# Optimization experiments

Measured on AMD Instinct MI355X. Metric: run time of the kernel, lower is better.

Reference implementation:

```python
import jax, jax.numpy as jnp
import numpy as np

N_NODES = 100000


def gcn_conv(x, W, b, src, tgt, n_nodes):
    """PyG GCNConv: add self-loops, symmetric deg^-1/2 normalization, then aggregate."""
    xw = x @ W  # [N, out]
    # degree including self-loop (edge weights are all 1)
    deg = jnp.zeros((n_nodes,), dtype=x.dtype).at[tgt].add(1.0) + 1.0
    dinv = deg ** -0.5
    norm = dinv[src] * dinv[tgt]  # [E]
    agg = jax.ops.segment_sum(xw[src] * norm[:, None], tgt, num_segments=n_nodes)
    # self-loop contribution: norm_ii = dinv_i^2
    return agg + xw * (dinv ** 2)[:, None] + b


def setup_inputs() -> dict:
    key = jax.random.key(0)
    ks = jax.random.split(key, 9)
    d_in, d_hid, d_out = 128, 128, 64
    x = jax.random.normal(ks[0], (N_NODES, d_in), dtype=jnp.float32)
    edge_index = jax.random.randint(ks[1], (2, 200000), 0, N_NODES)
    pos_edge_index = jax.random.randint(ks[2], (2, 500000), 0, N_NODES)
    s = lambda k, shape, fan: jax.random.normal(k, shape, dtype=jnp.float32) / np.sqrt(fan)
    return {
        "x": x,
        "edge_index": edge_index,
        "pos_edge_index": pos_edge_index,
        "W_init": s(ks[3], (d_in, d_in), d_in),
        "b_init": jnp.zeros((d_in,), dtype=jnp.float32),
        "W1": s(ks[4], (d_in, d_hid), d_in),
        "b1": jnp.zeros((d_hid,), dtype=jnp.float32),
        "W2": s(ks[5], (d_hid, d_out), d_hid),
        "b2": jnp.zeros((d_out,), dtype=jnp.float32),
    }


def reference(x, edge_index, pos_edge_index, W_init, b_init, W1, b1, W2, b2):
    n = x.shape[0]
    src, tgt = pos_edge_index[0], pos_edge_index[1]
    h = x @ W_init + b_init                      # init_linear
    h = gcn_conv(h, W1, b1, src, tgt, n)         # conv1
    h = jax.nn.relu(h)
    h = gcn_conv(h, W2, b2, src, tgt, n)         # conv2
    # edge dot-product scoring (use_bilinear=False)
    logits = jnp.sum(h[edge_index[0]] * h[edge_index[1]], axis=-1)  # [E_pred]
    return logits
```

## Files before the change

### kernel.cpp

```cpp
#include <hip/hip_runtime.h>


typedef __attribute__((ext_vector_type(8))) short short8;
typedef __attribute__((ext_vector_type(4))) float f32x4;

__device__ __forceinline__ ushort f2bf(float v) {
    unsigned u = __float_as_uint(v);
    return (ushort)((u + 0x7FFFu + ((u >> 16) & 1u)) >> 16);
}
__device__ __forceinline__ float bf2f(ushort b) {
    return __uint_as_float(((unsigned)b) << 16);
}
__device__ __forceinline__ void split2(float v, ushort& h, ushort& l) {
    unsigned u = __float_as_uint(v);
    unsigned hb = (u + 0x7FFFu + ((u >> 16) & 1u)) & 0xFFFF0000u;
    h = (ushort)(hb >> 16);
    l = f2bf(v - __uint_as_float(hb));
}

__global__ void zero_ints_kernel(int* __restrict__ p, int n) {
    int i = blockIdx.x * blockDim.x + threadIdx.x;
    if (i < n) p[i] = 0;
}
__global__ void hist_kernel(const int* __restrict__ tgt, int* __restrict__ counts, int e) {
    int i = blockIdx.x * blockDim.x + threadIdx.x;
    if (i < e) atomicAdd(&counts[tgt[i]], 1);
}
__global__ __launch_bounds__(256)
void scan1_kernel(const int* __restrict__ counts, int* __restrict__ rowptr,
                  int* __restrict__ bsum, float* __restrict__ dinv, int n)
{
    __shared__ int sdata[256];
    const int t = threadIdx.x;
    const int base = blockIdx.x * 1024 + t * 4;
    int v[4];
#pragma unroll
    for (int i = 0; i < 4; i++) v[i] = (base + i < n) ? counts[base + i] : 0;
#pragma unroll
    for (int i = 0; i < 4; i++)
        if (base + i < n) dinv[base + i] = 1.0f / sqrtf((float)(v[i] + 1));
    int tsum = v[0] + v[1] + v[2] + v[3];
    sdata[t] = tsum;
    __syncthreads();
    for (int off = 1; off < 256; off <<= 1) {
        int x = (t >= off) ? sdata[t - off] : 0;
        __syncthreads();
        if (t >= off) sdata[t] += x;
        __syncthreads();
    }
    if (t == 255) bsum[blockIdx.x] = sdata[255];
    int run = sdata[t] - tsum;
#pragma unroll
    for (int i = 0; i < 4; i++) {
        if (base + i < n) rowptr[base + i] = run;
        run += v[i];
    }
}
__global__ __launch_bounds__(256)
void scan2_kernel(int* __restrict__ bsum, int nb)
{
    __shared__ int sdata[256];
    const int t = threadIdx.x;
    int v = (t < nb) ? bsum[t] : 0;
    sdata[t] = v;
    __syncthreads();
    for (int off = 1; off < 256; off <<= 1) {
        int x = (t >= off) ? sdata[t - off] : 0;
        __syncthreads();
        if (t >= off) sdata[t] += x;
        __syncthreads();
    }
    if (t < nb) bsum[t] = sdata[t] - v;
}
__global__ void scan3_kernel(int* __restrict__ rowptr, const int* __restrict__ bsum,
                             int n, int e_total)
{
    int i = blockIdx.x * blockDim.x + threadIdx.x;
    if (i < n) rowptr[i] += bsum[i >> 10];
    if (i == 0) rowptr[n] = e_total;
}
__global__ void scatter_kernel(const int* __restrict__ src, const int* __restrict__ tgt,
                               const float* __restrict__ dinv, const int* __restrict__ rowptr,
                               int* __restrict__ cursor, int2* __restrict__ ew, int e)
{
    int i = blockIdx.x * blockDim.x + threadIdx.x;
    if (i >= e) return;
    int s = src[i], t = tgt[i];
    int p = rowptr[t] + atomicAdd(&cursor[t], 1);
    ew[p] = make_int2(s, __float_as_int(dinv[s] * dinv[t]));
}

__global__ void wtrans_all_kernel(const float* __restrict__ Wi, const float* __restrict__ W1,
                                  const float* __restrict__ W2,
                                  ushort* __restrict__ Ti, ushort* __restrict__ T1,
                                  ushort* __restrict__ T2)
{
    int o = blockIdx.x * blockDim.x + threadIdx.x;
    if (o < 16384) {
        int c = o >> 7, k = o & 127;
        Ti[o] = f2bf(Wi[(size_t)k * 128 + c]);
    } else if (o < 32768) {
        int p = o - 16384;
        int c = p >> 7, k = p & 127;
        T1[p] = f2bf(W1[(size_t)k * 128 + c]);
    } else if (o < 40960) {
        int p = o - 32768;
        int c = p >> 7, k = p & 127;
        T2[p] = f2bf(W2[(size_t)k * 64 + c]);
    }
}

__global__ __launch_bounds__(256)
void fused_gemm01_kernel(const float* __restrict__ x,
                         const ushort* __restrict__ WTi, const ushort* __restrict__ WT1,
                         const float* __restrict__ bias, ushort* __restrict__ xw1, int M)
{
    __shared__ ushort raw[36864];
    ushort (*H0h)[128][8] = (ushort(*)[128][8])raw;
    ushort (*H0l)[128][8] = (ushort(*)[128][8])(raw + 16384);
    ushort (*Bs)[128][8]  = (ushort(*)[128][8])(raw + 32768);

    const int tid = threadIdx.x;
    const int row0 = blockIdx.x * 128;
    const int wv = tid >> 6;
    const int l  = tid & 63;
    const int lr = l & 15;
    const int lk = l >> 4;

    f32x4 acc0[8], acc1[8];
#pragma unroll
    for (int n = 0; n < 8; ++n) {
        acc0[n] = (f32x4){0.f, 0.f, 0.f, 0.f};
        acc1[n] = (f32x4){0.f, 0.f, 0.f, 0.f};
    }

    for (int kk = 0; kk < 128; kk += 32) {
        {
            const int r  = tid >> 1;
            const int kh = tid & 1;
            const int gr = row0 + r;
            float f[16];
            if (gr < M) {
                const float4* p = (const float4*)(x + (size_t)gr * 128 + kk + kh * 16);
                float4 q0 = p[0], q1 = p[1], q2 = p[2], q3 = p[3];
                f[0]=q0.x; f[1]=q0.y; f[2]=q0.z; f[3]=q0.w;
                f[4]=q1.x; f[5]=q1.y; f[6]=q1.z; f[7]=q1.w;
                f[8]=q2.x; f[9]=q2.y; f[10]=q2.z; f[11]=q2.w;
                f[12]=q3.x; f[13]=q3.y; f[14]=q3.z; f[15]=q3.w;
            } else {
#pragma unroll
                for (int j = 0; j < 16; j++) f[j] = 0.f;
            }
#pragma unroll
            for (int uu = 0; uu < 2; ++uu) {
                short8 hv, lv;
#pragma unroll
                for (int j = 0; j < 8; ++j) {
                    ushort h, lo;
                    split2(f[8 * uu + j], h, lo);
                    hv[j] = (short)h; lv[j] = (short)lo;
                }
                *(short8*)&H0h[2 * kh + uu][r][0] = hv;
                *(short8*)&H0l[2 * kh + uu][r][0] = lv;
            }
        }
        {
#pragma unroll
            for (int u = 0; u < 2; ++u) {
                const int unit = tid * 2 + u;
                const int c   = unit >> 2;
                const int kgl = unit & 3;
                *(short8*)&Bs[kgl][c][0] = *(const short8*)(WTi + (size_t)c * 128 + kk + 8 * kgl);
            }
        }
        __syncthreads();
        short8 ah0 = *(const short8*)&H0h[lk][wv * 32 + lr][0];
        short8 ah1 = *(const short8*)&H0h[lk][wv * 32 + 16 + lr][0];
        short8 al0 = *(const short8*)&H0l[lk][wv * 32 + lr][0];
        short8 al1 = *(const short8*)&H0l[lk][wv * 32 + 16 + lr][0];
#pragma unroll
        for (int n = 0; n < 8; ++n) {
            short8 bh = *(const short8*)&Bs[lk][n * 16 + lr][0];
            acc0[n] = __builtin_amdgcn_mfma_f32_16x16x32_bf16(bh, ah0, acc0[n], 0, 0, 0);
            acc1[n] = __builtin_amdgcn_mfma_f32_16x16x32_bf16(bh, ah1, acc1[n], 0, 0, 0);
            acc0[n] = __builtin_amdgcn_mfma_f32_16x16x32_bf16(bh, al0, acc0[n], 0, 0, 0);
            acc1[n] = __builtin_amdgcn_mfma_f32_16x16x32_bf16(bh, al1, acc1[n], 0, 0, 0);
        }
        __syncthreads();
    }

#pragma unroll
    for (int n = 0; n < 8; ++n) {
        const float4 b4 = *(const float4*)(bias + n * 16 + 4 * lk);
        const float bb[4] = {b4.x, b4.y, b4.z, b4.w};
        const int ks = 2 * n + (lk >> 1);
        const int jo = (lk & 1) * 4;
#pragma unroll
        for (int half = 0; half < 2; ++half) {
            const int m = wv * 32 + 16 * half + lr;
            uint2 uh, ul;
            unsigned hw[4], lw[4];
#pragma unroll
            for (int r = 0; r < 4; ++r) {
                ushort h, lo;
                split2((half ? acc1[n][r] : acc0[n][r]) + bb[r], h, lo);
                hw[r] = h; lw[r] = lo;
            }
            uh.x = hw[0] | (hw[1] << 16); uh.y = hw[2] | (hw[3] << 16);
            ul.x = lw[0] | (lw[1] << 16); ul.y = lw[2] | (lw[3] << 16);
            *(uint2*)&H0h[ks][m][jo] = uh;
            *(uint2*)&H0l[ks][m][jo] = ul;
        }
    }
    __syncthreads();

#pragma unroll
    for (int n = 0; n < 8; ++n) {
        acc0[n] = (f32x4){0.f, 0.f, 0.f, 0.f};
        acc1[n] = (f32x4){0.f, 0.f, 0.f, 0.f};
    }
    for (int kk = 0; kk < 4; ++kk) {
        {
#pragma unroll
            for (int u = 0; u < 2; ++u) {
                const int unit = tid * 2 + u;
                const int c   = unit >> 2;
                const int kgl = unit & 3;
                *(short8*)&Bs[kgl][c][0] = *(const short8*)(WT1 + (size_t)c * 128 + kk * 32 + 8 * kgl);
            }
        }
        __syncthreads();
        short8 ah0 = *(const short8*)&H0h[kk * 4 + lk][wv * 32 + lr][0];
        short8 ah1 = *(const short8*)&H0h[kk * 4 + lk][wv * 32 + 16 + lr][0];
        short8 al0 = *(const short8*)&H0l[kk * 4 + lk][wv * 32 + lr][0];
        short8 al1 = *(const short8*)&H0l[kk * 4 + lk][wv * 32 + 16 + lr][0];
#pragma unroll
        for (int n = 0; n < 8; ++n) {
            short8 bh = *(const short8*)&Bs[lk][n * 16 + lr][0];
            acc0[n] = __builtin_amdgcn_mfma_f32_16x16x32_bf16(bh, ah0, acc0[n], 0, 0, 0);
            acc1[n] = __builtin_amdgcn_mfma_f32_16x16x32_bf16(bh, ah1, acc1[n], 0, 0, 0);
            acc0[n] = __builtin_amdgcn_mfma_f32_16x16x32_bf16(bh, al0, acc0[n], 0, 0, 0);
            acc1[n] = __builtin_amdgcn_mfma_f32_16x16x32_bf16(bh, al1, acc1[n], 0, 0, 0);
        }
        __syncthreads();
    }

#pragma unroll
    for (int n = 0; n < 8; ++n) {
#pragma unroll
        for (int half = 0; half < 2; ++half) {
            const int m = row0 + wv * 32 + 16 * half + lr;
            if (m < M) {
                uint2 u;
                const f32x4 a = half ? acc1[n] : acc0[n];
                u.x = (unsigned)f2bf(a[0]) | ((unsigned)f2bf(a[1]) << 16);
                u.y = (unsigned)f2bf(a[2]) | ((unsigned)f2bf(a[3]) << 16);
                *(uint2*)(xw1 + (size_t)m * 128 + n * 16 + 4 * lk) = u;
            }
        }
    }
}

__global__ __launch_bounds__(256)
void gemm2_kernel(const ushort* __restrict__ Ap, const ushort* __restrict__ WT2,
                  ushort* __restrict__ xw2, int M)
{
    __shared__ ushort Ah[4][128][8];
    __shared__ ushort Bs[4][64][8];

    const int tid = threadIdx.x;
    const int row0 = blockIdx.x * 128;
    const int wv = tid >> 6;
    const int l  = tid & 63;
    const int lr = l & 15;
    const int lk = l >> 4;

    f32x4 acc0[4], acc1[4];
#pragma unroll
    for (int n = 0; n < 4; ++n) {
        acc0[n] = (f32x4){0.f, 0.f, 0.f, 0.f};
        acc1[n] = (f32x4){0.f, 0.f, 0.f, 0.f};
    }

    for (int kk = 0; kk < 128; kk += 32) {
        {
            const int r  = tid >> 1;
            const int kh = tid & 1;
            const int gr = row0 + r;
            short8 h0, h1;
            if (gr < M) {
                const size_t o = (size_t)gr * 128 + kk + kh * 16;
                h0 = *(const short8*)(Ap + o);
                h1 = *(const short8*)(Ap + o + 8);
            } else {
#pragma unroll
                for (int j = 0; j < 8; j++) { h0[j] = 0; h1[j] = 0; }
            }
            *(short8*)&Ah[2 * kh + 0][r][0] = h0;
            *(short8*)&Ah[2 * kh + 1][r][0] = h1;
        }
        {
            const int c   = tid >> 2;
            const int kgl = tid & 3;
            *(short8*)&Bs[kgl][c][0] = *(const short8*)(WT2 + (size_t)c * 128 + kk + 8 * kgl);
        }
        __syncthreads();
        short8 ah0 = *(const short8*)&Ah[lk][wv * 32 + lr][0];
        short8 ah1 = *(const short8*)&Ah[lk][wv * 32 + 16 + lr][0];
#pragma unroll
        for (int n = 0; n < 4; ++n) {
            short8 bh = *(const short8*)&Bs[lk][n * 16 + lr][0];
            acc0[n] = __builtin_amdgcn_mfma_f32_16x16x32_bf16(bh, ah0, acc0[n], 0, 0, 0);
            acc1[n] = __builtin_amdgcn_mfma_f32_16x16x32_bf16(bh, ah1, acc1[n], 0, 0, 0);
        }
        __syncthreads();
    }

#pragma unroll
    for (int n = 0; n < 4; ++n) {
#pragma unroll
        for (int half = 0; half < 2; ++half) {
            const int m = row0 + wv * 32 + 16 * half + lr;
            if (m < M) {
                uint2 u;
                const f32x4 a = half ? acc1[n] : acc0[n];
                u.x = (unsigned)f2bf(a[0]) | ((unsigned)f2bf(a[1]) << 16);
                u.y = (unsigned)f2bf(a[2]) | ((unsigned)f2bf(a[3]) << 16);
                *(uint2*)(xw2 + (size_t)m * 64 + n * 16 + 4 * lk) = u;
            }
        }
    }
}

__global__ __launch_bounds__(256)
void gather1_kernel(const ushort* __restrict__ xw, const float* __restrict__ dinv,
                    const int* __restrict__ rowptr, const int2* __restrict__ ew,
                    const float* __restrict__ bias, ushort* __restrict__ outp, int n)
{
    const int node = blockIdx.x * 4 + (threadIdx.x >> 6);
    const int lane = threadIdx.x & 63;
    if (node >= n) return;
    const float dt = dinv[node];
    int j = rowptr[node];
    const int j1 = rowptr[node + 1];

    const unsigned self = *(const unsigned*)(xw + (size_t)node * 128 + 2 * lane);
    const float c = dt * dt;
    float accx = fmaf(__uint_as_float(self << 16), c, bias[2 * lane]);
    float accy = fmaf(__uint_as_float(self & 0xFFFF0000u), c, bias[2 * lane + 1]);

    for (; j + 3 < j1; j += 4) {
        const int2 p0 = ew[j], p1 = ew[j + 1], p2 = ew[j + 2], p3 = ew[j + 3];
        const unsigned v0 = *(const unsigned*)(xw + (size_t)p0.x * 128 + 2 * lane);
        const unsigned v1 = *(const unsigned*)(xw + (size_t)p1.x * 128 + 2 * lane);
        const unsigned v2 = *(const unsigned*)(xw + (size_t)p2.x * 128 + 2 * lane);
        const unsigned v3 = *(const unsigned*)(xw + (size_t)p3.x * 128 + 2 * lane);
        const float w0 = __int_as_float(p0.y), w1 = __int_as_float(p1.y);
        const float w2 = __int_as_float(p2.y), w3 = __int_as_float(p3.y);
        accx = fmaf(__uint_as_float(v0 << 16), w0, accx);
        accy = fmaf(__uint_as_float(v0 & 0xFFFF0000u), w0, accy);
        accx = fmaf(__uint_as_float(v1 << 16), w1, accx);
        accy = fmaf(__uint_as_float(v1 & 0xFFFF0000u), w1, accy);
        accx = fmaf(__uint_as_float(v2 << 16), w2, accx);
        accy = fmaf(__uint_as_float(v2 & 0xFFFF0000u), w2, accy);
        accx = fmaf(__uint_as_float(v3 << 16), w3, accx);
        accy = fmaf(__uint_as_float(v3 & 0xFFFF0000u), w3, accy);
    }
    for (; j < j1; ++j) {
        const int2 p0 = ew[j];
        const unsigned v0 = *(const unsigned*)(xw + (size_t)p0.x * 128 + 2 * lane);
        const float w0 = __int_as_float(p0.y);
        accx = fmaf(__uint_as_float(v0 << 16), w0, accx);
        accy = fmaf(__uint_as_float(v0 & 0xFFFF0000u), w0, accy);
    }

    const float rx = fmaxf(accx, 0.f);
    const float ry = fmaxf(accy, 0.f);
    *(unsigned*)(outp + (size_t)node * 128 + 2 * lane) =
        (unsigned)f2bf(rx) | ((unsigned)f2bf(ry) << 16);
}

__global__ __launch_bounds__(256)
void gather2_kernel(const ushort* __restrict__ xw, const float* __restrict__ dinv,
                    const int* __restrict__ rowptr, const int2* __restrict__ ew,
                    const float* __restrict__ bias, ushort* __restrict__ out, int n)
{
    const int node = blockIdx.x * 4 + (threadIdx.x >> 6);
    const int lane = threadIdx.x & 63;
    if (node >= n) return;
    const float dt = dinv[node];
    int j = rowptr[node];
    const int j1 = rowptr[node + 1];

    float acc = fmaf(bf2f(xw[(size_t)node * 64 + lane]), dt * dt, bias[lane]);
    for (; j + 3 < j1; j += 4) {
        const int2 p0 = ew[j], p1 = ew[j + 1], p2 = ew[j + 2], p3 = ew[j + 3];
        const float v0 = bf2f(xw[(size_t)p0.x * 64 + lane]);
        const float v1 = bf2f(xw[(size_t)p1.x * 64 + lane]);
        const float v2 = bf2f(xw[(size_t)p2.x * 64 + lane]);
        const float v3 = bf2f(xw[(size_t)p3.x * 64 + lane]);
        acc = fmaf(v0, __int_as_float(p0.y), acc);
        acc = fmaf(v1, __int_as_float(p1.y), acc);
        acc = fmaf(v2, __int_as_float(p2.y), acc);
        acc = fmaf(v3, __int_as_float(p3.y), acc);
    }
    for (; j < j1; ++j) {
        const int2 p0 = ew[j];
        acc = fmaf(bf2f(xw[(size_t)p0.x * 64 + lane]), __int_as_float(p0.y), acc);
    }
    out[(size_t)node * 64 + lane] = f2bf(acc);
}

__global__ void score_kernel(const ushort* __restrict__ h, const int* __restrict__ ea,
                             const int* __restrict__ eb, float* __restrict__ out, int E)
{
    long long gid = (long long)blockIdx.x * blockDim.x + threadIdx.x;
    int e = (int)(gid >> 3);
    int l = (int)(gid & 7);
    if (e >= E) return;
    int a = ea[e], b = eb[e];
    uint4 ua = *(const uint4*)(h + (size_t)a * 64 + 8 * l);
    uint4 ub = *(const uint4*)(h + (size_t)b * 64 + 8 * l);
    float s;
    s  = __uint_as_float(ua.x << 16)         * __uint_as_float(ub.x << 16);
    s += __uint_as_float(ua.x & 0xFFFF0000u) * __uint_as_float(ub.x & 0xFFFF0000u);
    s += __uint_as_float(ua.y << 16)         * __uint_as_float(ub.y << 16);
    s += __uint_as_float(ua.y & 0xFFFF0000u) * __uint_as_float(ub.y & 0xFFFF0000u);
    s += __uint_as_float(ua.z << 16)         * __uint_as_float(ub.z << 16);
    s += __uint_as_float(ua.z & 0xFFFF0000u) * __uint_as_float(ub.z & 0xFFFF0000u);
    s += __uint_as_float(ua.w << 16)         * __uint_as_float(ub.w << 16);
    s += __uint_as_float(ua.w & 0xFFFF0000u) * __uint_as_float(ub.w & 0xFFFF0000u);
    s += __shfl_xor(s, 4);
    s += __shfl_xor(s, 2);
    s += __shfl_xor(s, 1);
    if (l == 0) out[e] = s;
}

extern "C" void kernel_launch(void* const* d_in, const int* in_sizes, int n_in,
                              void* d_out, int out_size, void* d_ws, size_t ws_size,
                              hipStream_t stream)
{
    const float* x              = (const float*)d_in[0];
    const int*   edge_index     = (const int*)d_in[1];
    const int*   pos_edge_index = (const int*)d_in[2];
    const float* W_init         = (const float*)d_in[3];
    const float* b_init         = (const float*)d_in[4];
    const float* W1             = (const float*)d_in[5];
    const float* b1             = (const float*)d_in[6];
    const float* W2             = (const float*)d_in[7];
    const float* b2             = (const float*)d_in[8];
    float* out = (float*)d_out;

    const int N     = in_sizes[0] / 128;
    const int Epred = in_sizes[1] / 2;
    const int E     = in_sizes[2] / 2;

    const int* src = pos_edge_index;
    const int* tgt = pos_edge_index + E;
    const int* ea  = edge_index;
    const int* eb  = edge_index + Epred;

    int2*   ew   = (int2*)d_ws;
    ushort* regA = (ushort*)(ew + E);
    ushort* regB = regA + (size_t)N * 128;
    float*  dinv = (float*)(regB + (size_t)N * 128);
    int*   counts = (int*)(dinv + N);
    int*   cursor = counts + N;
    int*   rowptr = cursor + N;
    int*   bsum   = rowptr + N + 2;
    ushort* WTi = (ushort*)(((uintptr_t)(bsum + 256) + 15) & ~(uintptr_t)15);
    ushort* WT1 = WTi + 16384;
    ushort* WT2 = WT1 + 16384;

    ushort* xw1 = regA;
    ushort* r1  = regB;
    ushort* xw2 = regA;
    ushort* h2  = regB;

    const int BLK = 256;
    const int nb  = (N + 1023) / 1024;
    const int gemm_grid = (N + 127) / 128;

    zero_ints_kernel<<<(2 * N + BLK - 1) / BLK, BLK, 0, stream>>>(counts, 2 * N);
    hist_kernel<<<(E + BLK - 1) / BLK, BLK, 0, stream>>>(tgt, counts, E);
    scan1_kernel<<<nb, 256, 0, stream>>>(counts, rowptr, bsum, dinv, N);
    scan2_kernel<<<1, 256, 0, stream>>>(bsum, nb);
    scan3_kernel<<<(N + BLK - 1) / BLK, BLK, 0, stream>>>(rowptr, bsum, N, E);
    scatter_kernel<<<(E + BLK - 1) / BLK, BLK, 0, stream>>>(src, tgt, dinv, rowptr, cursor, ew, E);

    wtrans_all_kernel<<<160, BLK, 0, stream>>>(W_init, W1, W2, WTi, WT1, WT2);

    fused_gemm01_kernel<<<gemm_grid, BLK, 0, stream>>>(x, WTi, WT1, b_init, xw1, N);

    gather1_kernel<<<(N + 3) / 4, BLK, 0, stream>>>(xw1, dinv, rowptr, ew, b1, r1, N);

    gemm2_kernel<<<gemm_grid, BLK, 0, stream>>>(r1, WT2, xw2, N);

    gather2_kernel<<<(N + 3) / 4, BLK, 0, stream>>>(xw2, dinv, rowptr, ew, b2, h2, N);

    score_kernel<<<((long long)Epred * 8 + BLK - 1) / BLK, BLK, 0, stream>>>(
        h2, ea, eb, out, Epred);
}
```

Measured before the change: 196.9 us.

## Fuse conv1 gather, ReLU and second GEMM into one tiled kernel

Replaces the separate gather1 and gemm2 kernels with one kernel. Each block of 64 target nodes stages its CSR edges in shared memory and accumulates the neighbour aggregation into a bf16 shared tile. ReLU is applied by zeroing negative bf16 values, and the tile is then multiplied by W2 with MFMA, so the relu'd hidden activations never make a round trip through global memory. It also folds the counter zeroing into the weight-transpose kernel to save a launch. The cost is extra rounding, because per-segment partial sums are added into a bf16 tile, plus a binary search per edge and a slow fallback path for blocks with more than 1536 edges.

Result: faster. 192.6 us (-2.2%).

```diff
diff --git a/kernel.cpp b/kernel.cpp
--- a/kernel.cpp
+++ b/kernel.cpp
@@ -10,6 +10,11 @@
 }
 __device__ __forceinline__ float bf2f(ushort b) {
     return __uint_as_float(((unsigned)b) << 16);
+}
+__device__ __forceinline__ float bflo(unsigned u) { return __uint_as_float(u << 16); }
+__device__ __forceinline__ float bfhi(unsigned u) { return __uint_as_float(u & 0xFFFF0000u); }
+__device__ __forceinline__ unsigned packbf(float x, float y) {
+    return (unsigned)f2bf(x) | ((unsigned)f2bf(y) << 16);
 }
 __device__ __forceinline__ void split2(float v, ushort& h, ushort& l) {
     unsigned u = __float_as_uint(v);
@@ -18,84 +23,13 @@
     l = f2bf(v - __uint_as_float(hb));
 }
 
-__global__ void zero_ints_kernel(int* __restrict__ p, int n) {
-    int i = blockIdx.x * blockDim.x + threadIdx.x;
-    if (i < n) p[i] = 0;
-}
-__global__ void hist_kernel(const int* __restrict__ tgt, int* __restrict__ counts, int e) {
-    int i = blockIdx.x * blockDim.x + threadIdx.x;
-    if (i < e) atomicAdd(&counts[tgt[i]], 1);
-}
-__global__ __launch_bounds__(256)
-void scan1_kernel(const int* __restrict__ counts, int* __restrict__ rowptr,
-                  int* __restrict__ bsum, float* __restrict__ dinv, int n)
-{
-    __shared__ int sdata[256];
-    const int t = threadIdx.x;
-    const int base = blockIdx.x * 1024 + t * 4;
-    int v[4];
-#pragma unroll
-    for (int i = 0; i < 4; i++) v[i] = (base + i < n) ? counts[base + i] : 0;
-#pragma unroll
-    for (int i = 0; i < 4; i++)
-        if (base + i < n) dinv[base + i] = 1.0f / sqrtf((float)(v[i] + 1));
-    int tsum = v[0] + v[1] + v[2] + v[3];
-    sdata[t] = tsum;
-    __syncthreads();
-    for (int off = 1; off < 256; off <<= 1) {
-        int x = (t >= off) ? sdata[t - off] : 0;
-        __syncthreads();
-        if (t >= off) sdata[t] += x;
-        __syncthreads();
-    }
-    if (t == 255) bsum[blockIdx.x] = sdata[255];
-    int run = sdata[t] - tsum;
-#pragma unroll
-    for (int i = 0; i < 4; i++) {
-        if (base + i < n) rowptr[base + i] = run;
-        run += v[i];
-    }
-}
-__global__ __launch_bounds__(256)
-void scan2_kernel(int* __restrict__ bsum, int nb)
-{
-    __shared__ int sdata[256];
-    const int t = threadIdx.x;
-    int v = (t < nb) ? bsum[t] : 0;
-    sdata[t] = v;
-    __syncthreads();
-    for (int off = 1; off < 256; off <<= 1) {
-        int x = (t >= off) ? sdata[t - off] : 0;
-        __syncthreads();
-        if (t >= off) sdata[t] += x;
-        __syncthreads();
-    }
-    if (t < nb) bsum[t] = sdata[t] - v;
-}
-__global__ void scan3_kernel(int* __restrict__ rowptr, const int* __restrict__ bsum,
-                             int n, int e_total)
-{
-    int i = blockIdx.x * blockDim.x + threadIdx.x;
-    if (i < n) rowptr[i] += bsum[i >> 10];
-    if (i == 0) rowptr[n] = e_total;
-}
-__global__ void scatter_kernel(const int* __restrict__ src, const int* __restrict__ tgt,
-                               const float* __restrict__ dinv, const int* __restrict__ rowptr,
-                               int* __restrict__ cursor, int2* __restrict__ ew, int e)
-{
-    int i = blockIdx.x * blockDim.x + threadIdx.x;
-    if (i >= e) return;
-    int s = src[i], t = tgt[i];
-    int p = rowptr[t] + atomicAdd(&cursor[t], 1);
-    ew[p] = make_int2(s, __float_as_int(dinv[s] * dinv[t]));
-}
-
-__global__ void wtrans_all_kernel(const float* __restrict__ Wi, const float* __restrict__ W1,
-                                  const float* __restrict__ W2,
-                                  ushort* __restrict__ Ti, ushort* __restrict__ T1,
-                                  ushort* __restrict__ T2)
+__global__ void prep_kernel(const float* __restrict__ Wi, const float* __restrict__ W1,
+                            const float* __restrict__ W2,
+                            ushort* __restrict__ Ti, ushort* __restrict__ T1,
+                            ushort* __restrict__ T2, int* __restrict__ zp, int ztot)
 {
     int o = blockIdx.x * blockDim.x + threadIdx.x;
+    if (o < ztot) zp[o] = 0;
     if (o < 16384) {
         int c = o >> 7, k = o & 127;
         Ti[o] = f2bf(Wi[(size_t)k * 128 + c]);
@@ -108,6 +42,74 @@
         int c = p >> 7, k = p & 127;
         T2[p] = f2bf(W2[(size_t)k * 64 + c]);
     }
+}
+
+__global__ void hist_kernel(const int* __restrict__ tgt, int* __restrict__ counts, int e) {
+    int i = blockIdx.x * blockDim.x + threadIdx.x;
+    if (i < e) atomicAdd(&counts[tgt[i]], 1);
+}
+__global__ __launch_bounds__(256)
+void scan1_kernel(const int* __restrict__ counts, int* __restrict__ rowptr,
+                  int* __restrict__ bsum, float* __restrict__ dinv, int n)
+{
+    __shared__ int sdata[256];
+    const int t = threadIdx.x;
+    const int base = blockIdx.x * 1024 + t * 4;
+    int v[4];
+#pragma unroll
+    for (int i = 0; i < 4; i++) v[i] = (base + i < n) ? counts[base + i] : 0;
+#pragma unroll
+    for (int i = 0; i < 4; i++)
+        if (base + i < n) dinv[base + i] = 1.0f / sqrtf((float)(v[i] + 1));
+    int tsum = v[0] + v[1] + v[2] + v[3];
+    sdata[t] = tsum;
+    __syncthreads();
+    for (int off = 1; off < 256; off <<= 1) {
+        int x = (t >= off) ? sdata[t - off] : 0;
+        __syncthreads();
+        if (t >= off) sdata[t] += x;
+        __syncthreads();
+    }
+    if (t == 255) bsum[blockIdx.x] = sdata[255];
+    int run = sdata[t] - tsum;
+#pragma unroll
+    for (int i = 0; i < 4; i++) {
+        if (base + i < n) rowptr[base + i] = run;
+        run += v[i];
+    }
+}
+__global__ __launch_bounds__(256)
+void scan2_kernel(int* __restrict__ bsum, int nb)
+{
+    __shared__ int sdata[256];
+    const int t = threadIdx.x;
+    int v = (t < nb) ? bsum[t] : 0;
+    sdata[t] = v;
+    __syncthreads();
+    for (int off = 1; off < 256; off <<= 1) {
+        int x = (t >= off) ? sdata[t - off] : 0;
+        __syncthreads();
+        if (t >= off) sdata[t] += x;
+        __syncthreads();
+    }
+    if (t < nb) bsum[t] = sdata[t] - v;
+}
+__global__ void scan3_kernel(int* __restrict__ rowptr, const int* __restrict__ bsum,
+                             int n, int e_total)
+{
+    int i = blockIdx.x * blockDim.x + threadIdx.x;
+    if (i < n) rowptr[i] += bsum[i >> 10];
+    if (i == 0) rowptr[n] = e_total;
+}
+__global__ void scatter_kernel(const int* __restrict__ src, const int* __restrict__ tgt,
+                               const float* __restrict__ dinv, const int* __restrict__ rowptr,
+                               int* __restrict__ cursor, int2* __restrict__ ew, int e)
+{
+    int i = blockIdx.x * blockDim.x + threadIdx.x;
+    if (i >= e) return;
+    int s = src[i], t = tgt[i];
+    int p = rowptr[t] + atomicAdd(&cursor[t], 1);
+    ew[p] = make_int2(s, __float_as_int(dinv[s] * dinv[t]));
 }
 
 __global__ __launch_bounds__(256)
@@ -261,123 +263,155 @@
     }
 }
 
+#define C1_CAP 1536
+
+__device__ __forceinline__ void tile_add(unsigned* p, float ax, float ay) {
+    unsigned old = *p;
+    *p = packbf(bflo(old) + ax, bfhi(old) + ay);
+}
+
 __global__ __launch_bounds__(256)
-void gemm2_kernel(const ushort* __restrict__ Ap, const ushort* __restrict__ WT2,
-                  ushort* __restrict__ xw2, int M)
-{
-    __shared__ ushort Ah[4][128][8];
-    __shared__ ushort Bs[4][64][8];
-
-    const int tid = threadIdx.x;
-    const int row0 = blockIdx.x * 128;
-    const int wv = tid >> 6;
-    const int l  = tid & 63;
-    const int lr = l & 15;
-    const int lk = l >> 4;
-
-    f32x4 acc0[4], acc1[4];
-#pragma unroll
-    for (int n = 0; n < 4; ++n) {
-        acc0[n] = (f32x4){0.f, 0.f, 0.f, 0.f};
-        acc1[n] = (f32x4){0.f, 0.f, 0.f, 0.f};
-    }
-
-    for (int kk = 0; kk < 128; kk += 32) {
-        {
-            const int r  = tid >> 1;
-            const int kh = tid & 1;
-            const int gr = row0 + r;
-            short8 h0, h1;
-            if (gr < M) {
-                const size_t o = (size_t)gr * 128 + kk + kh * 16;
-                h0 = *(const short8*)(Ap + o);
-                h1 = *(const short8*)(Ap + o + 8);
-            } else {
-#pragma unroll
-                for (int j = 0; j < 8; j++) { h0[j] = 0; h1[j] = 0; }
-            }
-            *(short8*)&Ah[2 * kh + 0][r][0] = h0;
-            *(short8*)&Ah[2 * kh + 1][r][0] = h1;
-        }
-        {
-            const int c   = tid >> 2;
-            const int kgl = tid & 3;
-            *(short8*)&Bs[kgl][c][0] = *(const short8*)(WT2 + (size_t)c * 128 + kk + 8 * kgl);
-        }
-        __syncthreads();
-        short8 ah0 = *(const short8*)&Ah[lk][wv * 32 + lr][0];
-        short8 ah1 = *(const short8*)&Ah[lk][wv * 32 + 16 + lr][0];
+void conv1_fused_kernel(const ushort* __restrict__ xw1, const float* __restrict__ dinv,
+                        const int* __restrict__ rowptr, const int2* __restrict__ ew,
+                        const float* __restrict__ b1, const ushort* __restrict__ WT2,
+                        ushort* __restrict__ xw2, int N)
+{
+    __shared__ ushort tile[16][65][8];
+    __shared__ int2 sew[C1_CAP];
+    __shared__ int srp[65];
+
+    const int tid  = threadIdx.x;
+    const int n0   = blockIdx.x * 64;
+    const int nc   = min(64, N - n0);
+    const int wv   = tid >> 6;
+    const int lane = tid & 63;
+
+    if (tid <= nc) srp[tid] = rowptr[n0 + tid];
+    __syncthreads();
+    const int e0   = srp[0];
+    const int etot = srp[nc] - e0;
+    const int ecap = min(etot, C1_CAP);
+
+    for (int i = tid; i < ecap; i += 256) {
+        int2 d = ew[e0 + i];
+        int idx = e0 + i;
+        int lo = 0, hi = nc - 1;
+        while (lo < hi) { int mid = (lo + hi + 1) >> 1; if (srp[mid] <= idx) lo = mid; else hi = mid - 1; }
+        sew[i] = make_int2((d.x & 0xFFFFF) | (lo << 20), d.y);
+    }
+
+    const float bb0 = b1[2 * lane];
+    const float bb1 = b1[2 * lane + 1];
+    const int  kg = lane >> 2;
+    const int  jj = (2 * lane) & 7;
+    unsigned* tbase = (unsigned*)&tile[kg][0][jj];
+    for (int r = wv; r < 64; r += 4) {
+        float vx = 0.f, vy = 0.f;
+        if (r < nc) {
+            unsigned u = *(const unsigned*)(xw1 + (size_t)(n0 + r) * 128 + 2 * lane);
+            float dt = dinv[n0 + r];
+            float cc = dt * dt;
+            vx = fmaf(bflo(u), cc, bb0);
+            vy = fmaf(bfhi(u), cc, bb1);
+        }
+        tbase[r * 4] = packbf(vx, vy);
+    }
+    __syncthreads();
+
+    const int nlo = wv * 16;
+    if (nlo < nc) {
+        const int nhi = min(nlo + 16, nc);
+        int i = srp[nlo] - e0;
+        const int iend_all = srp[nhi] - e0;
+        const int iend = min(iend_all, ecap);
+        float ax = 0.f, ay = 0.f;
+        int cur = -1;
+
+        for (; i + 8 <= iend; i += 8) {
+            int2 d[8];
+#pragma unroll
+            for (int u = 0; u < 8; ++u) d[u] = sew[i + u];
+            unsigned v[8];
+#pragma unroll
+            for (int u = 0; u < 8; ++u)
+                v[u] = *(const unsigned*)(xw1 + (size_t)(((unsigned)d[u].x) & 0xFFFFFu) * 128 + 2 * lane);
+#pragma unroll
+            for (int u = 0; u < 8; ++u) {
+                const int tg = (int)(((unsigned)d[u].x) >> 20);
+                if (tg != cur) {
+                    if (cur >= 0) tile_add(tbase + cur * 4, ax, ay);
+                    cur = tg; ax = 0.f; ay = 0.f;
+                }
+                const float w = __int_as_float(d[u].y);
+                ax = fmaf(bflo(v[u]), w, ax);
+                ay = fmaf(bfhi(v[u]), w, ay);
+            }
+        }
+        for (; i < iend; ++i) {
+            int2 d = sew[i];
+            unsigned v = *(const unsigned*)(xw1 + (size_t)(((unsigned)d.x) & 0xFFFFFu) * 128 + 2 * lane);
+            const int tg = (int)(((unsigned)d.x) >> 20);
+            if (tg != cur) {
+                if (cur >= 0) tile_add(tbase + cur * 4, ax, ay);
+                cur = tg; ax = 0.f; ay = 0.f;
+            }
+            const float w = __int_as_float(d.y);
+            ax = fmaf(bflo(v), w, ax);
+            ay = fmaf(bfhi(v), w, ay);
+        }
+        if (cur >= 0) tile_add(tbase + cur * 4, ax, ay);
+
+        if (iend_all > ecap) {
+            for (int nn = nlo; nn < nhi; ++nn) {
+                int lo2 = max(srp[nn] - e0, ecap);
+                int hi2 = srp[nn + 1] - e0;
+                if (lo2 < hi2) {
+                    ax = 0.f; ay = 0.f;
+                    for (int t = lo2; t < hi2; ++t) {
+                        int2 d = ew[e0 + t];
+                        unsigned v = *(const unsigned*)(xw1 + (size_t)d.x * 128 + 2 * lane);
+                        const float w = __int_as_float(d.y);
+                        ax = fmaf(bflo(v), w, ax);
+                        ay = fmaf(bfhi(v), w, ay);
+                    }
+                    tile_add(tbase + nn * 4, ax, ay);
+                }
+            }
+        }
+    }
+    __syncthreads();
+
+    const int lr = lane & 15;
+    const int lk = lane >> 4;
+    f32x4 acc[4];
+#pragma unroll
+    for (int n = 0; n < 4; ++n) acc[n] = (f32x4){0.f, 0.f, 0.f, 0.f};
+
+    for (int kt = 0; kt < 4; ++kt) {
+        short8 ah = *(const short8*)&tile[kt * 4 + lk][wv * 16 + lr][0];
+#pragma unroll
+        for (int j = 0; j < 8; ++j) {
+            ushort vv = (ushort)ah[j];
+            ah[j] = (short)((vv & 0x8000u) ? 0 : vv);
+        }
 #pragma unroll
         for (int n = 0; n < 4; ++n) {
-            short8 bh = *(const short8*)&Bs[lk][n * 16 + lr][0];
-            acc0[n] = __builtin_amdgcn_mfma_f32_16x16x32_bf16(bh, ah0, acc0[n], 0, 0, 0);
-            acc1[n] = __builtin_amdgcn_mfma_f32_16x16x32_bf16(bh, ah1, acc1[n], 0, 0, 0);
-        }
-        __syncthreads();
-    }
-
-#pragma unroll
-    for (int n = 0; n < 4; ++n) {
-#pragma unroll
-        for (int half = 0; half < 2; ++half) {
-            const int m = row0 + wv * 32 + 16 * half + lr;
-            if (m < M) {
-                uint2 u;
-                const f32x4 a = half ? acc1[n] : acc0[n];
-                u.x = (unsigned)f2bf(a[0]) | ((unsigned)f2bf(a[1]) << 16);
-                u.y = (unsigned)f2bf(a[2]) | ((unsigned)f2bf(a[3]) << 16);
-                *(uint2*)(xw2 + (size_t)m * 64 + n * 16 + 4 * lk) = u;
-            }
-        }
-    }
-}
-
-__global__ __launch_bounds__(256)
-void gather1_kernel(const ushort* __restrict__ xw, const float* __restrict__ dinv,
-                    const int* __restrict__ rowptr, const int2* __restrict__ ew,
-                    const float* __restrict__ bias, ushort* __restrict__ outp, int n)
-{
-    const int node = blockIdx.x * 4 + (threadIdx.x >> 6);
-    const int lane = threadIdx.x & 63;
-    if (node >= n) return;
-    const float dt = dinv[node];
-    int j = rowptr[node];
-    const int j1 = rowptr[node + 1];
-
-    const unsigned self = *(const unsigned*)(xw + (size_t)node * 128 + 2 * lane);
-    const float c = dt * dt;
-    float accx = fmaf(__uint_as_float(self << 16), c, bias[2 * lane]);
-    float accy = fmaf(__uint_as_float(self & 0xFFFF0000u), c, bias[2 * lane + 1]);
-
-    for (; j + 3 < j1; j += 4) {
-        const int2 p0 = ew[j], p1 = ew[j + 1], p2 = ew[j + 2], p3 = ew[j + 3];
-        const unsigned v0 = *(const unsigned*)(xw + (size_t)p0.x * 128 + 2 * lane);
-        const unsigned v1 = *(const unsigned*)(xw + (size_t)p1.x * 128 + 2 * lane);
-        const unsigned v2 = *(const unsigned*)(xw + (size_t)p2.x * 128 + 2 * lane);
-        const unsigned v3 = *(const unsigned*)(xw + (size_t)p3.x * 128 + 2 * lane);
-        const float w0 = __int_as_float(p0.y), w1 = __int_as_float(p1.y);
-        const float w2 = __int_as_float(p2.y), w3 = __int_as_float(p3.y);
-        accx = fmaf(__uint_as_float(v0 << 16), w0, accx);
-        accy = fmaf(__uint_as_float(v0 & 0xFFFF0000u), w0, accy);
-        accx = fmaf(__uint_as_float(v1 << 16), w1, accx);
-        accy = fmaf(__uint_as_float(v1 & 0xFFFF0000u), w1, accy);
-        accx = fmaf(__uint_as_float(v2 << 16), w2, accx);
-        accy = fmaf(__uint_as_float(v2 & 0xFFFF0000u), w2, accy);
-        accx = fmaf(__uint_as_float(v3 << 16), w3, accx);
-        accy = fmaf(__uint_as_float(v3 & 0xFFFF0000u), w3, accy);
-    }
-    for (; j < j1; ++j) {
-        const int2 p0 = ew[j];
-        const unsigned v0 = *(const unsigned*)(xw + (size_t)p0.x * 128 + 2 * lane);
-        const float w0 = __int_as_float(p0.y);
-        accx = fmaf(__uint_as_float(v0 << 16), w0, accx);
-        accy = fmaf(__uint_as_float(v0 & 0xFFFF0000u), w0, accy);
-    }
-
-    const float rx = fmaxf(accx, 0.f);
-    const float ry = fmaxf(accy, 0.f);
-    *(unsigned*)(outp + (size_t)node * 128 + 2 * lane) =
-        (unsigned)f2bf(rx) | ((unsigned)f2bf(ry) << 16);
+            short8 bh = *(const short8*)(WT2 + (size_t)(n * 16 + lr) * 128 + kt * 32 + lk * 8);
+            acc[n] = __builtin_amdgcn_mfma_f32_16x16x32_bf16(bh, ah, acc[n], 0, 0, 0);
+        }
+    }
+
+    const int ml = wv * 16 + lr;
+    if (ml < nc) {
+        const size_t m = (size_t)(n0 + ml);
+#pragma unroll
+        for (int n = 0; n < 4; ++n) {
+            uint2 u;
+            u.x = (unsigned)f2bf(acc[n][0]) | ((unsigned)f2bf(acc[n][1]) << 16);
+            u.y = (unsigned)f2bf(acc[n][2]) | ((unsigned)f2bf(acc[n][3]) << 16);
+            *(uint2*)(xw2 + m * 64 + n * 16 + 4 * lk) = u;
+        }
+    }
 }
 
 __global__ __launch_bounds__(256)
@@ -473,28 +507,25 @@
     ushort* WT2 = WT1 + 16384;
 
     ushort* xw1 = regA;
-    ushort* r1  = regB;
-    ushort* xw2 = regA;
-    ushort* h2  = regB;
+    ushort* xw2 = regB;
+    ushort* h2  = regB + (size_t)N * 64;
 
     const int BLK = 256;
     const int nb  = (N + 1023) / 1024;
-    const int gemm_grid = (N + 127) / 128;
-
-    zero_ints_kernel<<<(2 * N + BLK - 1) / BLK, BLK, 0, stream>>>(counts, 2 * N);
+
+    prep_kernel<<<(2 * N + BLK - 1) / BLK, BLK, 0, stream>>>(
+        W_init, W1, W2, WTi, WT1, WT2, counts, 2 * N);
+
     hist_kernel<<<(E + BLK - 1) / BLK, BLK, 0, stream>>>(tgt, counts, E);
     scan1_kernel<<<nb, 256, 0, stream>>>(counts, rowptr, bsum, dinv, N);
     scan2_kernel<<<1, 256, 0, stream>>>(bsum, nb);
     scan3_kernel<<<(N + BLK - 1) / BLK, BLK, 0, stream>>>(rowptr, bsum, N, E);
     scatter_kernel<<<(E + BLK - 1) / BLK, BLK, 0, stream>>>(src, tgt, dinv, rowptr, cursor, ew, E);
 
-    wtrans_all_kernel<<<160, BLK, 0, stream>>>(W_init, W1, W2, WTi, WT1, WT2);
-
-    fused_gemm01_kernel<<<gemm_grid, BLK, 0, stream>>>(x, WTi, WT1, b_init, xw1, N);
-
-    gather1_kernel<<<(N + 3) / 4, BLK, 0, stream>>>(xw1, dinv, rowptr, ew, b1, r1, N);
-
-    gemm2_kernel<<<gemm_grid, BLK, 0, stream>>>(r1, WT2, xw2, N);
+    fused_gemm01_kernel<<<(N + 127) / 128, BLK, 0, stream>>>(x, WTi, WT1, b_init, xw1, N);
+
+    conv1_fused_kernel<<<(N + 63) / 64, BLK, 0, stream>>>(
+        xw1, dinv, rowptr, ew, b1, WT2, xw2, N);
 
     gather2_kernel<<<(N + 3) / 4, BLK, 0, stream>>>(xw2, dinv, rowptr, ew, b2, h2, N);
 
```
